# Optimization experiments

Measured on AMD Instinct MI355X. Metric: run time of the kernel, lower is better.

## Reference

```python
import jax, jax.numpy as jnp
import numpy as np

N = 8192
IN_F = 128
N_HID = 64
OUT_F = 128
NEG = -9.0e15


def _xavier(key, shape, gain=1.414):
    fan_in, fan_out = shape
    a = gain * np.sqrt(6.0 / (fan_in + fan_out))
    return jax.random.uniform(key, shape, jnp.float32, -a, a)


def setup_inputs() -> dict:
    key = jax.random.key(0)
    k_h, k_adj, k_ws, k_wt, k_wc = jax.random.split(key, 5)
    h = jax.random.normal(k_h, (N, IN_F), dtype=jnp.float32)
    adj = jax.random.randint(k_adj, (N, N), 0, 2, dtype=jnp.int32)
    Ws = _xavier(k_ws, (IN_F, N_HID))
    Wt = _xavier(k_wt, (IN_F, N_HID))
    Wc = _xavier(k_wc, (IN_F, OUT_F))
    return {"h": h, "adj": adj, "Ws": Ws, "Wt": Wt, "Wc": Wc}


def reference(h, adj, Ws, Wt, Wc):
    # Whs: [N, H], Wht: [N, H]
    Whs = h @ Ws
    Wht = h @ Wt
    # e: [N, N] dense attention scores
    e = jnp.einsum("nh,mh->nm", Whs, Wht)
    z = jnp.where(adj > 0, e, jnp.asarray(NEG, e.dtype))
    alpha = jax.nn.softmax(z, axis=-1)  # [N, N]
    Whc = h @ Wc                        # [N, OUT_F]
    h_prime = alpha @ Whc               # [N, OUT_F]
    return h_prime
```

## Files before the change

### kernel.cpp

```cpp
#include <hip/hip_runtime.h>


#define NN 8192
#define INF_ 128
#define NHID 64
#define OUTF 128
#define NEGC -9.0e15f

typedef unsigned short u16;
typedef __attribute__((ext_vector_type(8))) short bf16x8;
typedef __attribute__((ext_vector_type(4))) float f32x4;
typedef __attribute__((ext_vector_type(4))) int i32x4;
typedef __attribute__((ext_vector_type(4))) unsigned u32x4;

static __device__ __forceinline__ u16 f2bf(float x) {
  union { float f; unsigned u; } v; v.f = x;
  unsigned lsb = (v.u >> 16) & 1u;
  v.u += 0x7fffu + lsb;
  return (u16)(v.u >> 16);
}
static __device__ __forceinline__ float bf2f(u16 h) {
  union { float f; unsigned u; } v; v.u = ((unsigned)h) << 16;
  return v.f;
}
static __device__ __forceinline__ f32x4 mfma16(bf16x8 a, bf16x8 b, f32x4 c) {
  return __builtin_amdgcn_mfma_f32_16x16x32_bf16(a, b, c, 0, 0, 0);
}

__global__ __launch_bounds__(256) void proj_kernel(
    const float* __restrict__ h, const float* __restrict__ Ws,
    const float* __restrict__ Wt, const float* __restrict__ Wc,
    u16* __restrict__ whs_hi, u16* __restrict__ whs_lo,
    u16* __restrict__ wht_hi, u16* __restrict__ wht_lo,
    u16* __restrict__ whcT) {
  __shared__ f32x4 hbuf[8][32];
  const int tid = threadIdx.x;
  const int r0 = blockIdx.x * 8;
  hbuf[tid >> 5][tid & 31] =
      reinterpret_cast<const f32x4*>(h)[(size_t)r0 * 32 + tid];
  __syncthreads();

  float acc[8];
#pragma unroll
  for (int r = 0; r < 8; ++r) acc[r] = 0.f;

  if (tid < 128) {
    const float* W = (tid < 64) ? (Ws + tid) : (Wt + (tid - 64));
#pragma unroll 4
    for (int k4 = 0; k4 < 32; ++k4) {
      float w0 = W[(k4 * 4 + 0) * NHID];
      float w1 = W[(k4 * 4 + 1) * NHID];
      float w2 = W[(k4 * 4 + 2) * NHID];
      float w3 = W[(k4 * 4 + 3) * NHID];
#pragma unroll
      for (int r = 0; r < 8; ++r) {
        f32x4 hv = hbuf[r][k4];
        acc[r] += hv.x * w0 + hv.y * w1 + hv.z * w2 + hv.w * w3;
      }
    }
    const int col = tid & 63;
    u16* hi = (tid < 64) ? whs_hi : wht_hi;
    u16* lo = (tid < 64) ? whs_lo : wht_lo;
#pragma unroll
    for (int r = 0; r < 8; ++r) {
      float v = acc[r];
      u16 hb = f2bf(v);
      hi[(size_t)(r0 + r) * NHID + col] = hb;
      lo[(size_t)(r0 + r) * NHID + col] = f2bf(v - bf2f(hb));
    }
  } else {
    const int col = tid - 128;
    const float* W = Wc + col;
#pragma unroll 4
    for (int k4 = 0; k4 < 32; ++k4) {
      float w0 = W[(k4 * 4 + 0) * OUTF];
      float w1 = W[(k4 * 4 + 1) * OUTF];
      float w2 = W[(k4 * 4 + 2) * OUTF];
      float w3 = W[(k4 * 4 + 3) * OUTF];
#pragma unroll
      for (int r = 0; r < 8; ++r) {
        f32x4 hv = hbuf[r][k4];
        acc[r] += hv.x * w0 + hv.y * w1 + hv.z * w2 + hv.w * w3;
      }
    }
    union { u16 s[8]; u32x4 v; } pk;
#pragma unroll
    for (int r = 0; r < 8; ++r) pk.s[r] = f2bf(acc[r]);
    *reinterpret_cast<u32x4*>(whcT + (size_t)col * NN + r0) = pk.v;
  }
}

__global__ __launch_bounds__(256, 2) void attn_kernel(
    const u16* __restrict__ whs_hi, const u16* __restrict__ whs_lo,
    const u16* __restrict__ wht_hi, const u16* __restrict__ wht_lo,
    const u16* __restrict__ whcT, const int* __restrict__ adj,
    float* __restrict__ Opart, float* __restrict__ mpart,
    float* __restrict__ lpart, float* __restrict__ out,
    int iters, int cshift, int final_write) {
  __shared__ __align__(16) u16 Bst[2][2][64 * 72];
  __shared__ __align__(16) u16 Wst[2][128 * 64];
  __shared__ __align__(16) u16 Pbuf[4][16][72];
  __shared__ __align__(16) u16 Mbuf[2][64][4];

  const int tid = threadIdx.x;
  const int w = tid >> 6;
  const int lane = tid & 63;
  const int q = lane >> 4;
  const int ln = lane & 15;
  const int chunk = blockIdx.x & ((1 << cshift) - 1);
  const int rb = blockIdx.x >> cshift;
  const int rowB = rb * 64;
  const int row0 = rowB + w * 16;

  const int bcol = tid >> 2;
  const int bsh = (tid >> 1) & 1;
  const int bkh = tid & 1;
  const u16* bg = (bsh ? wht_lo : wht_hi) + (size_t)bcol * NHID + bkh * 32;
  const int wocol = tid >> 1;
  const int wjh = tid & 1;
  const u16* wg = whcT + (size_t)wocol * NN + wjh * 32;
  const int wsw0 = ((2 * wjh + 0) ^ (wocol & 3)) * 16;
  const int wsw1 = ((2 * wjh + 1) ^ (wocol & 3)) * 16;
  const int arow = tid >> 2;
  const int agrp = tid & 3;
  const int* ag = adj + (size_t)(rowB + arow) * NN + agrp * 16;

  bf16x8 a_hi[2], a_lo[2];
#pragma unroll
  for (int kh = 0; kh < 2; ++kh) {
    a_hi[kh] = *reinterpret_cast<const bf16x8*>(
        whs_hi + (size_t)(row0 + ln) * NHID + kh * 32 + q * 8);
    a_lo[kh] = *reinterpret_cast<const bf16x8*>(
        whs_lo + (size_t)(row0 + ln) * NHID + kh * 32 + q * 8);
  }

  f32x4 oacc[8];
#pragma unroll
  for (int ot = 0; ot < 8; ++ot)
#pragma unroll
    for (int g = 0; g < 4; ++g) oacc[ot][g] = 0.f;

  float m_old[4], l_run[4];
#pragma unroll
  for (int g = 0; g < 4; ++g) { m_old[g] = -__builtin_inff(); l_run[g] = 0.f; }

  const int jbase = chunk * iters;

  {
    const size_t j0 = (size_t)jbase * 64;
    const u32x4* p = reinterpret_cast<const u32x4*>(bg + j0 * NHID);
    u32x4 b0 = p[0], b1 = p[1], b2 = p[2], b3 = p[3];
    const u32x4* pw = reinterpret_cast<const u32x4*>(wg + j0);
    u32x4 w0 = pw[0], w1 = pw[1], w2 = pw[2], w3 = pw[3];
    const i32x4* pa = reinterpret_cast<const i32x4*>(ag + j0);
    i32x4 a0 = __builtin_nontemporal_load(pa + 0);
    i32x4 a1 = __builtin_nontemporal_load(pa + 1);
    i32x4 a2 = __builtin_nontemporal_load(pa + 2);
    i32x4 a3 = __builtin_nontemporal_load(pa + 3);
    u32x4* d = reinterpret_cast<u32x4*>(&Bst[0][bsh][bcol * 72 + bkh * 32]);
    d[0] = b0; d[1] = b1; d[2] = b2; d[3] = b3;
    u32x4* e0 = reinterpret_cast<u32x4*>(&Wst[0][wocol * 64 + wsw0]);
    e0[0] = w0; e0[1] = w1;
    u32x4* e1 = reinterpret_cast<u32x4*>(&Wst[0][wocol * 64 + wsw1]);
    e1[0] = w2; e1[1] = w3;
    unsigned mw = 0;
    mw |= (a0.x>0?1u:0u)<<0  | (a0.y>0?1u:0u)<<1  | (a0.z>0?1u:0u)<<2  | (a0.w>0?1u:0u)<<3;
    mw |= (a1.x>0?1u:0u)<<4  | (a1.y>0?1u:0u)<<5  | (a1.z>0?1u:0u)<<6  | (a1.w>0?1u:0u)<<7;
    mw |= (a2.x>0?1u:0u)<<8  | (a2.y>0?1u:0u)<<9  | (a2.z>0?1u:0u)<<10 | (a2.w>0?1u:0u)<<11;
    mw |= (a3.x>0?1u:0u)<<12 | (a3.y>0?1u:0u)<<13 | (a3.z>0?1u:0u)<<14 | (a3.w>0?1u:0u)<<15;
    Mbuf[0][arow][agrp] = (u16)mw;
  }
  __syncthreads();

  for (int jt = 0; jt < iters; ++jt) {
    const int buf = jt & 1;

    u32x4 sb0, sb1, sb2, sb3, sw0, sw1, sw2, sw3;
    i32x4 ad0, ad1, ad2, ad3;
    if (jt + 1 < iters) {
      const size_t j1 = (size_t)(jbase + jt + 1) * 64;
      const u32x4* p = reinterpret_cast<const u32x4*>(bg + j1 * NHID);
      sb0 = p[0]; sb1 = p[1]; sb2 = p[2]; sb3 = p[3];
      const u32x4* pw = reinterpret_cast<const u32x4*>(wg + j1);
      sw0 = pw[0]; sw1 = pw[1]; sw2 = pw[2]; sw3 = pw[3];
      const i32x4* pa = reinterpret_cast<const i32x4*>(ag + j1);
      ad0 = __builtin_nontemporal_load(pa + 0);
      ad1 = __builtin_nontemporal_load(pa + 1);
      ad2 = __builtin_nontemporal_load(pa + 2);
      ad3 = __builtin_nontemporal_load(pa + 3);
    }

    unsigned mk01[4], mk23[4];
#pragma unroll
    for (int g = 0; g < 4; ++g) {
      const unsigned* mrow = reinterpret_cast<const unsigned*>(
          &Mbuf[buf][w * 16 + q * 4 + g][0]);
      mk01[g] = mrow[0];
      mk23[g] = mrow[1];
    }

    const u16* Bh = &Bst[buf][0][0];
    const u16* Bl = &Bst[buf][1][0];
    float s[4][4];
#pragma unroll
    for (int nt = 0; nt < 4; ++nt) {
      const int base = (nt * 16 + ln) * 72 + q * 8;
      bf16x8 bh0 = *reinterpret_cast<const bf16x8*>(&Bh[base]);
      bf16x8 bh1 = *reinterpret_cast<const bf16x8*>(&Bh[base + 32]);
      bf16x8 bl0 = *reinterpret_cast<const bf16x8*>(&Bl[base]);
      bf16x8 bl1 = *reinterpret_cast<const bf16x8*>(&Bl[base + 32]);
      f32x4 sa;
#pragma unroll
      for (int g = 0; g < 4; ++g) sa[g] = 0.f;
      sa = mfma16(a_lo[0], bh0, sa);
      sa = mfma16(a_hi[0], bl0, sa);
      sa = mfma16(a_hi[0], bh0, sa);
      sa = mfma16(a_lo[1], bh1, sa);
      sa = mfma16(a_hi[1], bl1, sa);
      sa = mfma16(a_hi[1], bh1, sa);
#pragma unroll
      for (int g = 0; g < 4; ++g) {
        unsigned wrd = (nt == 0) ? (mk01[g] & 0xffffu)
                     : (nt == 1) ? (mk01[g] >> 16)
                     : (nt == 2) ? (mk23[g] & 0xffffu)
                                 : (mk23[g] >> 16);
        s[nt][g] = ((wrd >> ln) & 1u) ? sa[g] : NEGC;
      }
    }

    float mr[4];
#pragma unroll
    for (int g = 0; g < 4; ++g)
      mr[g] = fmaxf(fmaxf(s[0][g], s[1][g]), fmaxf(s[2][g], s[3][g]));
#pragma unroll
    for (int msk = 1; msk <= 8; msk <<= 1)
#pragma unroll
      for (int g = 0; g < 4; ++g) mr[g] = fmaxf(mr[g], __shfl_xor(mr[g], msk));

    float mn[4], alpha[4], ps[4];
#pragma unroll
    for (int g = 0; g < 4; ++g) {
      mn[g] = fmaxf(m_old[g], mr[g]);
      alpha[g] = __expf(m_old[g] - mn[g]);
      m_old[g] = mn[g];
      ps[g] = 0.f;
    }
#pragma unroll
    for (int nt = 0; nt < 4; ++nt)
#pragma unroll
      for (int g = 0; g < 4; ++g) {
        float p = __expf(s[nt][g] - mn[g]);
        ps[g] += p;
        Pbuf[w][q * 4 + g][nt * 16 + ln] = f2bf(p);
      }
#pragma unroll
    for (int msk = 1; msk <= 8; msk <<= 1)
#pragma unroll
      for (int g = 0; g < 4; ++g) ps[g] += __shfl_xor(ps[g], msk);
#pragma unroll
    for (int g = 0; g < 4; ++g) l_run[g] = l_run[g] * alpha[g] + ps[g];
#pragma unroll
    for (int ot = 0; ot < 8; ++ot)
#pragma unroll
      for (int g = 0; g < 4; ++g) oacc[ot][g] *= alpha[g];

#pragma unroll
    for (int kh = 0; kh < 2; ++kh) {
      bf16x8 pa = *reinterpret_cast<const bf16x8*>(
          &Pbuf[w][ln][kh * 32 + q * 8]);
      const int c = kh * 2 + (q >> 1);
      const int sub = (q & 1) * 8;
#pragma unroll
      for (int ot = 0; ot < 8; ++ot) {
        const int ocol = ot * 16 + ln;
        bf16x8 wb = *reinterpret_cast<const bf16x8*>(
            &Wst[buf][ocol * 64 + ((c ^ (ocol & 3)) << 4) + sub]);
        oacc[ot] = mfma16(pa, wb, oacc[ot]);
      }
    }

    if (jt + 1 < iters) {
      const int nb = buf ^ 1;
      u32x4* d = reinterpret_cast<u32x4*>(&Bst[nb][bsh][bcol * 72 + bkh * 32]);
      d[0] = sb0; d[1] = sb1; d[2] = sb2; d[3] = sb3;
      u32x4* e0 = reinterpret_cast<u32x4*>(&Wst[nb][wocol * 64 + wsw0]);
      e0[0] = sw0; e0[1] = sw1;
      u32x4* e1 = reinterpret_cast<u32x4*>(&Wst[nb][wocol * 64 + wsw1]);
      e1[0] = sw2; e1[1] = sw3;
      unsigned mw = 0;
      mw |= (ad0.x>0?1u:0u)<<0  | (ad0.y>0?1u:0u)<<1  | (ad0.z>0?1u:0u)<<2  | (ad0.w>0?1u:0u)<<3;
      mw |= (ad1.x>0?1u:0u)<<4  | (ad1.y>0?1u:0u)<<5  | (ad1.z>0?1u:0u)<<6  | (ad1.w>0?1u:0u)<<7;
      mw |= (ad2.x>0?1u:0u)<<8  | (ad2.y>0?1u:0u)<<9  | (ad2.z>0?1u:0u)<<10 | (ad2.w>0?1u:0u)<<11;
      mw |= (ad3.x>0?1u:0u)<<12 | (ad3.y>0?1u:0u)<<13 | (ad3.z>0?1u:0u)<<14 | (ad3.w>0?1u:0u)<<15;
      Mbuf[buf ^ 1][arow][agrp] = (u16)mw;
    }
    __syncthreads();
  }

  if (final_write) {
#pragma unroll
    for (int ot = 0; ot < 8; ++ot)
#pragma unroll
      for (int g = 0; g < 4; ++g) {
        const int r = row0 + q * 4 + g;
        out[(size_t)r * OUTF + ot * 16 + ln] = oacc[ot][g] / l_run[g];
      }
  } else {
#pragma unroll
    for (int ot = 0; ot < 8; ++ot)
#pragma unroll
      for (int g = 0; g < 4; ++g) {
        const int r = row0 + q * 4 + g;
        Opart[((size_t)chunk * NN + r) * OUTF + ot * 16 + ln] = oacc[ot][g];
      }
    if (ln == 0) {
#pragma unroll
      for (int g = 0; g < 4; ++g) {
        const int r = row0 + q * 4 + g;
        mpart[chunk * NN + r] = m_old[g];
        lpart[chunk * NN + r] = l_run[g];
      }
    }
  }
}

__global__ __launch_bounds__(256) void combine_kernel(
    const float* __restrict__ Opart, const float* __restrict__ mpart,
    const float* __restrict__ lpart, float* __restrict__ out, int C) {
  const int idx = blockIdx.x * 256 + threadIdx.x;
  const int row = idx >> 7;
  float M = -__builtin_inff();
  for (int c = 0; c < C; ++c) M = fmaxf(M, mpart[c * NN + row]);
  float den = 0.f, num = 0.f;
  for (int c = 0; c < C; ++c) {
    float wgt = __expf(mpart[c * NN + row] - M);
    den += lpart[c * NN + row] * wgt;
    num += Opart[(size_t)c * NN * OUTF + idx] * wgt;
  }
  out[idx] = num / den;
}

extern "C" void kernel_launch(void* const* d_in, const int* in_sizes, int n_in,
                              void* d_out, int out_size, void* d_ws, size_t ws_size,
                              hipStream_t stream) {
  const float* h   = (const float*)d_in[0];
  const int*   adj = (const int*)d_in[1];
  const float* Ws  = (const float*)d_in[2];
  const float* Wt  = (const float*)d_in[3];
  const float* Wc  = (const float*)d_in[4];
  float* out = (float*)d_out;

  char* ws = (char*)d_ws;
  const size_t MB = 1024 * 1024;
  u16* whs_hi = (u16*)(ws);
  u16* whs_lo = (u16*)(ws + 1 * MB);
  u16* wht_hi = (u16*)(ws + 2 * MB);
  u16* wht_lo = (u16*)(ws + 3 * MB);
  u16* whcT   = (u16*)(ws + 4 * MB);
  float* mpart = (float*)(ws + 6 * MB);
  float* lpart = (float*)(ws + 6 * MB + 256 * 1024);
  float* Opart = (float*)(ws + 6 * MB + 512 * 1024);

  int C = 4, cshift = 2;
  if (6 * MB + 512 * 1024 + (size_t)C * NN * OUTF * sizeof(float) > ws_size) {
    C = 1; cshift = 0;
  }
  const int final_write = (C == 1) ? 1 : 0;
  const int iters = NN / (C * 64);

  proj_kernel<<<NN / 8, 256, 0, stream>>>(h, Ws, Wt, Wc, whs_hi, whs_lo,
                                          wht_hi, wht_lo, whcT);
  attn_kernel<<<(NN / 64) * C, 256, 0, stream>>>(
      whs_hi, whs_lo, wht_hi, wht_lo, whcT, adj, Opart, mpart, lpart, out,
      iters, cshift, final_write);
  if (!final_write)
    combine_kernel<<<NN * OUTF / 256, 256, 0, stream>>>(Opart, mpart, lpart,
                                                        out, C);
}
```

Measured before the change: 450.9 us.

## Halve attention key tile to 32 and raise occupancy with more column chunks

Shrinks the per-iteration key/value tile in the flash-style attention kernel from 64 to 32 columns. This halves the shared-memory staging buffers and packs the adjacency mask into bytes instead of 16-bit words. Launch bounds go from 2 to 4 blocks per EU, and the column split grows from 4 to 8 chunks, so more blocks stay resident to hide memory latency. The trade-offs are a barrier every 32 columns instead of every 64, shorter contiguous adjacency loads per row, tighter register limits that could cause spills, and a bigger partial-result buffer for the combine kernel to read.

```diff
diff --git a/kernel.cpp b/kernel.cpp
--- a/kernel.cpp
+++ b/kernel.cpp
@@ -8,6 +8,7 @@
 #define NEGC -9.0e15f
 
 typedef unsigned short u16;
+typedef unsigned char u8;
 typedef __attribute__((ext_vector_type(8))) short bf16x8;
 typedef __attribute__((ext_vector_type(4))) float f32x4;
 typedef __attribute__((ext_vector_type(4))) int i32x4;
@@ -90,17 +91,17 @@
   }
 }
 
-__global__ __launch_bounds__(256, 2) void attn_kernel(
+__global__ __launch_bounds__(256, 4) void attn_kernel(
     const u16* __restrict__ whs_hi, const u16* __restrict__ whs_lo,
     const u16* __restrict__ wht_hi, const u16* __restrict__ wht_lo,
     const u16* __restrict__ whcT, const int* __restrict__ adj,
     float* __restrict__ Opart, float* __restrict__ mpart,
     float* __restrict__ lpart, float* __restrict__ out,
     int iters, int cshift, int final_write) {
-  __shared__ __align__(16) u16 Bst[2][2][64 * 72];
-  __shared__ __align__(16) u16 Wst[2][128 * 64];
-  __shared__ __align__(16) u16 Pbuf[4][16][72];
-  __shared__ __align__(16) u16 Mbuf[2][64][4];
+  __shared__ __align__(16) u16 Bst[2][2][32 * 72];
+  __shared__ __align__(16) u16 Wst[2][128 * 32];
+  __shared__ __align__(16) u16 Pbuf[4][16][40];
+  __shared__ __align__(16) u8  Mbuf[2][64][4];
 
   const int tid = threadIdx.x;
   const int w = tid >> 6;
@@ -112,18 +113,18 @@
   const int rowB = rb * 64;
   const int row0 = rowB + w * 16;
 
-  const int bcol = tid >> 2;
-  const int bsh = (tid >> 1) & 1;
-  const int bkh = tid & 1;
-  const u16* bg = (bsh ? wht_lo : wht_hi) + (size_t)bcol * NHID + bkh * 32;
+  const int bcol = tid >> 3;
+  const int bsh = (tid >> 2) & 1;
+  const int bkq = tid & 3;
+  const u16* bg = (bsh ? wht_lo : wht_hi) + (size_t)bcol * NHID + bkq * 16;
   const int wocol = tid >> 1;
   const int wjh = tid & 1;
-  const u16* wg = whcT + (size_t)wocol * NN + wjh * 32;
-  const int wsw0 = ((2 * wjh + 0) ^ (wocol & 3)) * 16;
-  const int wsw1 = ((2 * wjh + 1) ^ (wocol & 3)) * 16;
+  const u16* wg = whcT + (size_t)wocol * NN + wjh * 16;
+  const int wsw0 = ((2 * wjh + 0) ^ (wocol & 3)) * 8;
+  const int wsw1 = ((2 * wjh + 1) ^ (wocol & 3)) * 8;
   const int arow = tid >> 2;
   const int agrp = tid & 3;
-  const int* ag = adj + (size_t)(rowB + arow) * NN + agrp * 16;
+  const int* ag = adj + (size_t)(rowB + arow) * NN + agrp * 8;
 
   bf16x8 a_hi[2], a_lo[2];
 #pragma unroll
@@ -147,63 +148,52 @@
   const int jbase = chunk * iters;
 
   {
-    const size_t j0 = (size_t)jbase * 64;
+    const size_t j0 = (size_t)jbase * 32;
     const u32x4* p = reinterpret_cast<const u32x4*>(bg + j0 * NHID);
-    u32x4 b0 = p[0], b1 = p[1], b2 = p[2], b3 = p[3];
+    u32x4 b0 = p[0], b1 = p[1];
     const u32x4* pw = reinterpret_cast<const u32x4*>(wg + j0);
-    u32x4 w0 = pw[0], w1 = pw[1], w2 = pw[2], w3 = pw[3];
+    u32x4 w0 = pw[0], w1 = pw[1];
     const i32x4* pa = reinterpret_cast<const i32x4*>(ag + j0);
     i32x4 a0 = __builtin_nontemporal_load(pa + 0);
     i32x4 a1 = __builtin_nontemporal_load(pa + 1);
-    i32x4 a2 = __builtin_nontemporal_load(pa + 2);
-    i32x4 a3 = __builtin_nontemporal_load(pa + 3);
-    u32x4* d = reinterpret_cast<u32x4*>(&Bst[0][bsh][bcol * 72 + bkh * 32]);
-    d[0] = b0; d[1] = b1; d[2] = b2; d[3] = b3;
-    u32x4* e0 = reinterpret_cast<u32x4*>(&Wst[0][wocol * 64 + wsw0]);
-    e0[0] = w0; e0[1] = w1;
-    u32x4* e1 = reinterpret_cast<u32x4*>(&Wst[0][wocol * 64 + wsw1]);
-    e1[0] = w2; e1[1] = w3;
+    u32x4* d = reinterpret_cast<u32x4*>(&Bst[0][bsh][bcol * 72 + bkq * 16]);
+    d[0] = b0; d[1] = b1;
+    *reinterpret_cast<u32x4*>(&Wst[0][wocol * 32 + wsw0]) = w0;
+    *reinterpret_cast<u32x4*>(&Wst[0][wocol * 32 + wsw1]) = w1;
     unsigned mw = 0;
-    mw |= (a0.x>0?1u:0u)<<0  | (a0.y>0?1u:0u)<<1  | (a0.z>0?1u:0u)<<2  | (a0.w>0?1u:0u)<<3;
-    mw |= (a1.x>0?1u:0u)<<4  | (a1.y>0?1u:0u)<<5  | (a1.z>0?1u:0u)<<6  | (a1.w>0?1u:0u)<<7;
-    mw |= (a2.x>0?1u:0u)<<8  | (a2.y>0?1u:0u)<<9  | (a2.z>0?1u:0u)<<10 | (a2.w>0?1u:0u)<<11;
-    mw |= (a3.x>0?1u:0u)<<12 | (a3.y>0?1u:0u)<<13 | (a3.z>0?1u:0u)<<14 | (a3.w>0?1u:0u)<<15;
-    Mbuf[0][arow][agrp] = (u16)mw;
+    mw |= (a0.x>0?1u:0u)<<0 | (a0.y>0?1u:0u)<<1 | (a0.z>0?1u:0u)<<2 | (a0.w>0?1u:0u)<<3;
+    mw |= (a1.x>0?1u:0u)<<4 | (a1.y>0?1u:0u)<<5 | (a1.z>0?1u:0u)<<6 | (a1.w>0?1u:0u)<<7;
+    Mbuf[0][arow][agrp] = (u8)mw;
   }
   __syncthreads();
 
   for (int jt = 0; jt < iters; ++jt) {
     const int buf = jt & 1;
 
-    u32x4 sb0, sb1, sb2, sb3, sw0, sw1, sw2, sw3;
-    i32x4 ad0, ad1, ad2, ad3;
+    u32x4 sb0, sb1, sw0, sw1;
+    i32x4 ad0, ad1;
     if (jt + 1 < iters) {
-      const size_t j1 = (size_t)(jbase + jt + 1) * 64;
+      const size_t j1 = (size_t)(jbase + jt + 1) * 32;
       const u32x4* p = reinterpret_cast<const u32x4*>(bg + j1 * NHID);
-      sb0 = p[0]; sb1 = p[1]; sb2 = p[2]; sb3 = p[3];
+      sb0 = p[0]; sb1 = p[1];
       const u32x4* pw = reinterpret_cast<const u32x4*>(wg + j1);
-      sw0 = pw[0]; sw1 = pw[1]; sw2 = pw[2]; sw3 = pw[3];
+      sw0 = pw[0]; sw1 = pw[1];
       const i32x4* pa = reinterpret_cast<const i32x4*>(ag + j1);
       ad0 = __builtin_nontemporal_load(pa + 0);
       ad1 = __builtin_nontemporal_load(pa + 1);
-      ad2 = __builtin_nontemporal_load(pa + 2);
-      ad3 = __builtin_nontemporal_load(pa + 3);
-    }
-
-    unsigned mk01[4], mk23[4];
-#pragma unroll
-    for (int g = 0; g < 4; ++g) {
-      const unsigned* mrow = reinterpret_cast<const unsigned*>(
+    }
+
+    unsigned mk[4];
+#pragma unroll
+    for (int g = 0; g < 4; ++g)
+      mk[g] = *reinterpret_cast<const unsigned*>(
           &Mbuf[buf][w * 16 + q * 4 + g][0]);
-      mk01[g] = mrow[0];
-      mk23[g] = mrow[1];
-    }
 
     const u16* Bh = &Bst[buf][0][0];
     const u16* Bl = &Bst[buf][1][0];
-    float s[4][4];
-#pragma unroll
-    for (int nt = 0; nt < 4; ++nt) {
+    float s[2][4];
+#pragma unroll
+    for (int nt = 0; nt < 2; ++nt) {
       const int base = (nt * 16 + ln) * 72 + q * 8;
       bf16x8 bh0 = *reinterpret_cast<const bf16x8*>(&Bh[base]);
       bf16x8 bh1 = *reinterpret_cast<const bf16x8*>(&Bh[base + 32]);
@@ -219,19 +209,13 @@
       sa = mfma16(a_hi[1], bl1, sa);
       sa = mfma16(a_hi[1], bh1, sa);
 #pragma unroll
-      for (int g = 0; g < 4; ++g) {
-        unsigned wrd = (nt == 0) ? (mk01[g] & 0xffffu)
-                     : (nt == 1) ? (mk01[g] >> 16)
-                     : (nt == 2) ? (mk23[g] & 0xffffu)
-                                 : (mk23[g] >> 16);
-        s[nt][g] = ((wrd >> ln) & 1u) ? sa[g] : NEGC;
-      }
+      for (int g = 0; g < 4; ++g)
+        s[nt][g] = ((mk[g] >> (nt * 16 + ln)) & 1u) ? sa[g] : NEGC;
     }
 
     float mr[4];
 #pragma unroll
-    for (int g = 0; g < 4; ++g)
-      mr[g] = fmaxf(fmaxf(s[0][g], s[1][g]), fmaxf(s[2][g], s[3][g]));
+    for (int g = 0; g < 4; ++g) mr[g] = fmaxf(s[0][g], s[1][g]);
 #pragma unroll
     for (int msk = 1; msk <= 8; msk <<= 1)
 #pragma unroll
@@ -246,7 +230,7 @@
       ps[g] = 0.f;
     }
 #pragma unroll
-    for (int nt = 0; nt < 4; ++nt)
+    for (int nt = 0; nt < 2; ++nt)
 #pragma unroll
       for (int g = 0; g < 4; ++g) {
         float p = __expf(s[nt][g] - mn[g]);
@@ -264,35 +248,27 @@
 #pragma unroll
       for (int g = 0; g < 4; ++g) oacc[ot][g] *= alpha[g];
 
-#pragma unroll
-    for (int kh = 0; kh < 2; ++kh) {
-      bf16x8 pa = *reinterpret_cast<const bf16x8*>(
-          &Pbuf[w][ln][kh * 32 + q * 8]);
-      const int c = kh * 2 + (q >> 1);
-      const int sub = (q & 1) * 8;
+    {
+      bf16x8 pa = *reinterpret_cast<const bf16x8*>(&Pbuf[w][ln][q * 8]);
 #pragma unroll
       for (int ot = 0; ot < 8; ++ot) {
         const int ocol = ot * 16 + ln;
         bf16x8 wb = *reinterpret_cast<const bf16x8*>(
-            &Wst[buf][ocol * 64 + ((c ^ (ocol & 3)) << 4) + sub]);
+            &Wst[buf][ocol * 32 + ((q ^ (ocol & 3)) << 3)]);
         oacc[ot] = mfma16(pa, wb, oacc[ot]);
       }
     }
 
     if (jt + 1 < iters) {
       const int nb = buf ^ 1;
-      u32x4* d = reinterpret_cast<u32x4*>(&Bst[nb][bsh][bcol * 72 + bkh * 32]);
-      d[0] = sb0; d[1] = sb1; d[2] = sb2; d[3] = sb3;
-      u32x4* e0 = reinterpret_cast<u32x4*>(&Wst[nb][wocol * 64 + wsw0]);
-      e0[0] = sw0; e0[1] = sw1;
-      u32x4* e1 = reinterpret_cast<u32x4*>(&Wst[nb][wocol * 64 + wsw1]);
-      e1[0] = sw2; e1[1] = sw3;
+      u32x4* d = reinterpret_cast<u32x4*>(&Bst[nb][bsh][bcol * 72 + bkq * 16]);
+      d[0] = sb0; d[1] = sb1;
+      *reinterpret_cast<u32x4*>(&Wst[nb][wocol * 32 + wsw0]) = sw0;
+      *reinterpret_cast<u32x4*>(&Wst[nb][wocol * 32 + wsw1]) = sw1;
       unsigned mw = 0;
-      mw |= (ad0.x>0?1u:0u)<<0  | (ad0.y>0?1u:0u)<<1  | (ad0.z>0?1u:0u)<<2  | (ad0.w>0?1u:0u)<<3;
-      mw |= (ad1.x>0?1u:0u)<<4  | (ad1.y>0?1u:0u)<<5  | (ad1.z>0?1u:0u)<<6  | (ad1.w>0?1u:0u)<<7;
-      mw |= (ad2.x>0?1u:0u)<<8  | (ad2.y>0?1u:0u)<<9  | (ad2.z>0?1u:0u)<<10 | (ad2.w>0?1u:0u)<<11;
-      mw |= (ad3.x>0?1u:0u)<<12 | (ad3.y>0?1u:0u)<<13 | (ad3.z>0?1u:0u)<<14 | (ad3.w>0?1u:0u)<<15;
-      Mbuf[buf ^ 1][arow][agrp] = (u16)mw;
+      mw |= (ad0.x>0?1u:0u)<<0 | (ad0.y>0?1u:0u)<<1 | (ad0.z>0?1u:0u)<<2 | (ad0.w>0?1u:0u)<<3;
+      mw |= (ad1.x>0?1u:0u)<<4 | (ad1.y>0?1u:0u)<<5 | (ad1.z>0?1u:0u)<<6 | (ad1.w>0?1u:0u)<<7;
+      Mbuf[nb][arow][agrp] = (u8)mw;
     }
     __syncthreads();
   }
@@ -361,12 +337,13 @@
   float* lpart = (float*)(ws + 6 * MB + 256 * 1024);
   float* Opart = (float*)(ws + 6 * MB + 512 * 1024);
 
-  int C = 4, cshift = 2;
-  if (6 * MB + 512 * 1024 + (size_t)C * NN * OUTF * sizeof(float) > ws_size) {
-    C = 1; cshift = 0;
+  int C = 8, cshift = 3;
+  while (C > 1 &&
+         6 * MB + 512 * 1024 + (size_t)C * NN * OUTF * sizeof(float) > ws_size) {
+    C >>= 1; cshift -= 1;
   }
   const int final_write = (C == 1) ? 1 : 0;
-  const int iters = NN / (C * 64);
+  const int iters = NN / (C * 32);
 
   proj_kernel<<<NN / 8, 256, 0, stream>>>(h, Ws, Wt, Wc, whs_hi, whs_lo,
                                           wht_hi, wht_lo, whcT);
```

Result: slower. 469.7 us (+4.2%).
